# Optimization experiments

Measured on AMD Instinct MI355X. Metric: run time of the kernel, lower is better.

The kernel has to match this reference:

```python
import jax, jax.numpy as jnp
import numpy as np

NB_SAMPLES = 16
GAMMA = 0.04       # also the noise_intensity passed to randomArgmax
ALPHA = 1.0
EPS = 1e-10


def setup_inputs() -> dict:
    key = jax.random.key(0)
    k1, k2, k3 = jax.random.split(key, 3)
    B, H, W, K = 8, 128, 128, 32
    zbuf = jax.random.normal(k1, (B, H, W, K), dtype=jnp.float32)
    prob_map = jax.random.uniform(k2, (B, H, W, K), dtype=jnp.float32)
    mask = jnp.ones((B, H, W, K), dtype=jnp.float32)
    zfar = jnp.ones((1,), dtype=jnp.float32)
    znear = jnp.zeros((1,), dtype=jnp.float32)
    # gaussian noise normally drawn inside randomArgmax.forward; made explicit for determinism
    noise = jax.random.normal(k3, (NB_SAMPLES, B, H, W, K + 1), dtype=jnp.float32)
    return {"zbuf": zbuf, "zfar": zfar, "znear": znear,
            "prob_map": prob_map, "mask": mask, "noise": noise}


def _random_argmax(z, noise, sigma):
    # z: [B,H,W,C]; noise: [S,B,H,W,C]
    C = z.shape[-1]
    z_pert = z[None] + sigma * noise                       # [S,B,H,W,C]
    idx = jnp.argmax(z_pert, axis=-1)                      # first-max, matches torch.max
    weights = jax.nn.one_hot(idx, C, dtype=z.dtype)        # [S,B,H,W,C]
    return weights.mean(axis=0)                            # [B,H,W,C]


def reference(zbuf, zfar, znear, prob_map, mask, noise):
    # inverse depth, masked
    z_inv = (zfar - zbuf) / (zfar - znear) * mask          # [B,H,W,K]
    z_inv_max = jnp.maximum(jnp.max(z_inv, axis=-1, keepdims=True), EPS)
    z_map = GAMMA / ALPHA * jnp.log(1e-12 + prob_map) + z_inv - z_inv_max
    bg = EPS - z_inv_max                                   # background channel [B,H,W,1]
    z_map = jnp.concatenate([z_map, bg], axis=-1)          # [B,H,W,K+1]
    return _random_argmax(z_map, noise, GAMMA)
```

## Files before the change

kernel.cpp:

```cpp
#include <hip/hip_runtime.h>


#define NPIX   (8 * 128 * 128)
#define KCH    32
#define CCH    33
#define SAMP   16
#define TPB    256
#define TILE   (TPB * CCH)

#define GLL16(gp, lp)                                                     \
    __builtin_amdgcn_global_load_lds(                                     \
        (const __attribute__((address_space(1))) void*)(gp),              \
        (__attribute__((address_space(3))) void*)(lp), 16, 0, 0)

__device__ __forceinline__ void stage_tile(const float* __restrict__ gsrc,
                                           float* ldst, int tid)
{
    #pragma unroll
    for (int j = 0; j < (TILE / 4) / TPB; ++j) {
        const int i = tid + j * TPB;
        GLL16(gsrc + 4 * i, ldst + 4 * i);
    }
    if (tid < (TILE / 4) - ((TILE / 4) / TPB) * TPB) {
        const int i = tid + ((TILE / 4) / TPB) * TPB;
        GLL16(gsrc + 4 * i, ldst + 4 * i);
    }
}

__global__ __launch_bounds__(TPB)
void gauss_agg_kernel(const float* __restrict__ zbuf,
                      const float* __restrict__ zfar_p,
                      const float* __restrict__ znear_p,
                      const float* __restrict__ prob,
                      const float* __restrict__ mask,
                      const float* __restrict__ noise,
                      float* __restrict__ out)
{
#pragma clang fp contract(off)
    __shared__ float lds[2 * TILE];
    const int tid = threadIdx.x;
    const int p0  = blockIdx.x * TPB;
    const size_t p = (size_t)p0 + tid;

    stage_tile(noise + ((size_t)0 * NPIX + p0) * CCH, lds, tid);

    const float zfar  = zfar_p[0];
    const float znear = znear_p[0];
    const float denom = zfar - znear;

    float zb[KCH], pm[KCH], mk[KCH];
    {
        const float4* zb4 = reinterpret_cast<const float4*>(zbuf + p * KCH);
        const float4* pm4 = reinterpret_cast<const float4*>(prob + p * KCH);
        const float4* mk4 = reinterpret_cast<const float4*>(mask + p * KCH);
        #pragma unroll
        for (int i = 0; i < KCH / 4; ++i) {
            float4 a = zb4[i], b = pm4[i], c = mk4[i];
            zb[4*i+0] = a.x; zb[4*i+1] = a.y; zb[4*i+2] = a.z; zb[4*i+3] = a.w;
            pm[4*i+0] = b.x; pm[4*i+1] = b.y; pm[4*i+2] = b.z; pm[4*i+3] = b.w;
            mk[4*i+0] = c.x; mk[4*i+1] = c.y; mk[4*i+2] = c.z; mk[4*i+3] = c.w;
        }
    }

    float z_inv[KCH];
    float zmax = 1e-10f;
    #pragma unroll
    for (int k = 0; k < KCH; ++k) {
        float zi = ((zfar - zb[k]) / denom) * mk[k];
        z_inv[k] = zi;
        zmax = fmaxf(zmax, zi);
    }

    float z_map[CCH];
    #pragma unroll
    for (int k = 0; k < KCH; ++k) {
        float lg = logf(1e-12f + pm[k]);
        z_map[k] = ((0.04f * lg) + z_inv[k]) - zmax;
    }
    z_map[KCH] = 1e-10f - zmax;

    int acc[CCH];
    #pragma unroll
    for (int c = 0; c < CCH; ++c) acc[c] = 0;

    __syncthreads();

    for (int s = 0; s < SAMP; ++s) {
        if (s + 1 < SAMP)
            stage_tile(noise + ((size_t)(s + 1) * NPIX + p0) * CCH,
                       lds + ((s + 1) & 1) * TILE, tid);

        const float* cur = lds + (s & 1) * TILE;
        const int base = tid * CCH;
        float best = z_map[0] + (0.04f * cur[base + 0]);
        int bi = 0;
        #pragma unroll
        for (int c = 1; c < CCH; ++c) {
            float v = z_map[c] + (0.04f * cur[base + c]);
            if (v > best) { best = v; bi = c; }
        }
        #pragma unroll
        for (int c = 0; c < CCH; ++c) acc[c] += (bi == c) ? 1 : 0;

        __syncthreads();
    }

    {
        const int base = tid * CCH;
        #pragma unroll
        for (int c = 0; c < CCH; ++c)
            lds[base + c] = (float)acc[c] * 0.0625f;
    }
    __syncthreads();
    {
        const float4* l4 = reinterpret_cast<const float4*>(lds);
        float4* o4 = reinterpret_cast<float4*>(out + (size_t)p0 * CCH);
        for (int i = tid; i < TILE / 4; i += TPB) o4[i] = l4[i];
    }
}

extern "C" void kernel_launch(void* const* d_in, const int* in_sizes, int n_in,
                              void* d_out, int out_size, void* d_ws, size_t ws_size,
                              hipStream_t stream)
{
    const float* zbuf  = (const float*)d_in[0];
    const float* zfar  = (const float*)d_in[1];
    const float* znear = (const float*)d_in[2];
    const float* prob  = (const float*)d_in[3];
    const float* mask  = (const float*)d_in[4];
    const float* noise = (const float*)d_in[5];
    float* out = (float*)d_out;

    dim3 grid(NPIX / TPB), block(TPB);
    gauss_agg_kernel<<<grid, block, 0, stream>>>(zbuf, zfar, znear, prob, mask,
                                                 noise, out);
}
```

Baseline: 408.6 us.

## Stage noise per wavefront and replace block barriers with vmcnt waits

Each wavefront now double-buffers only the noise slice for its own 64 pixels into its own LDS region, instead of the whole block staging a shared tile. This lets the per-sample `__syncthreads` be replaced by an explicit `s_waitcnt vmcnt(9)`, which waits only for the previous stage's async global-to-LDS loads. The aim is to remove block-wide stalls so waves progress independently and overlap loads with the argmax. The risk is that correctness depends on the exact count of outstanding vector-memory instructions per stage.

```diff
diff --git a/kernel.cpp b/kernel.cpp
--- a/kernel.cpp
+++ b/kernel.cpp
@@ -7,24 +7,40 @@
 #define SAMP   16
 #define TPB    256
 #define TILE   (TPB * CCH)
+#define WFLOATS (64 * CCH)
 
 #define GLL16(gp, lp)                                                     \
     __builtin_amdgcn_global_load_lds(                                     \
         (const __attribute__((address_space(1))) void*)(gp),              \
         (__attribute__((address_space(3))) void*)(lp), 16, 0, 0)
 
-__device__ __forceinline__ void stage_tile(const float* __restrict__ gsrc,
-                                           float* ldst, int tid)
+__device__ __forceinline__ void stage_wave(const float* __restrict__ gsrc,
+                                           float* ldst, int lane)
 {
     #pragma unroll
-    for (int j = 0; j < (TILE / 4) / TPB; ++j) {
-        const int i = tid + j * TPB;
-        GLL16(gsrc + 4 * i, ldst + 4 * i);
+    for (int j = 0; j < 8; ++j) {
+        const int f = j * 64 + lane;
+        GLL16(gsrc + 4 * f, ldst + 4 * f);
     }
-    if (tid < (TILE / 4) - ((TILE / 4) / TPB) * TPB) {
-        const int i = tid + ((TILE / 4) / TPB) * TPB;
-        GLL16(gsrc + 4 * i, ldst + 4 * i);
+    if (lane < 16) {
+        const int f = 512 + lane;
+        GLL16(gsrc + 4 * f, ldst + 4 * f);
     }
+}
+
+__device__ __forceinline__ void argmax_sample(const float* __restrict__ cur,
+                                              const float* __restrict__ z_map,
+                                              int* __restrict__ acc, int base)
+{
+    float best = z_map[0] + (0.04f * cur[base + 0]);
+    int bi = 0;
+    #pragma unroll
+    for (int c = 1; c < CCH; ++c) {
+        float v = z_map[c] + (0.04f * cur[base + c]);
+        if (v > best) { best = v; bi = c; }
+    }
+    #pragma unroll
+    for (int c = 0; c < CCH; ++c) acc[c] += (bi == c) ? 1 : 0;
 }
 
 __global__ __launch_bounds__(TPB)
@@ -38,11 +54,13 @@
 {
 #pragma clang fp contract(off)
     __shared__ float lds[2 * TILE];
-    const int tid = threadIdx.x;
-    const int p0  = blockIdx.x * TPB;
+    const int tid  = threadIdx.x;
+    const int lane = tid & 63;
+    const int wsl  = (tid >> 6) * WFLOATS;
+    const int p0   = blockIdx.x * TPB;
     const size_t p = (size_t)p0 + tid;
 
-    stage_tile(noise + ((size_t)0 * NPIX + p0) * CCH, lds, tid);
+    stage_wave(noise + ((size_t)0 * NPIX + p0) * CCH + wsl, lds + wsl, lane);
 
     const float zfar  = zfar_p[0];
     const float znear = znear_p[0];
@@ -83,33 +101,26 @@
     #pragma unroll
     for (int c = 0; c < CCH; ++c) acc[c] = 0;
 
-    __syncthreads();
+    const int base = tid * CCH - wsl;
 
-    for (int s = 0; s < SAMP; ++s) {
-        if (s + 1 < SAMP)
-            stage_tile(noise + ((size_t)(s + 1) * NPIX + p0) * CCH,
-                       lds + ((s + 1) & 1) * TILE, tid);
-
-        const float* cur = lds + (s & 1) * TILE;
-        const int base = tid * CCH;
-        float best = z_map[0] + (0.04f * cur[base + 0]);
-        int bi = 0;
-        #pragma unroll
-        for (int c = 1; c < CCH; ++c) {
-            float v = z_map[c] + (0.04f * cur[base + c]);
-            if (v > best) { best = v; bi = c; }
-        }
-        #pragma unroll
-        for (int c = 0; c < CCH; ++c) acc[c] += (bi == c) ? 1 : 0;
-
-        __syncthreads();
+    for (int s = 0; s < SAMP - 1; ++s) {
+        stage_wave(noise + ((size_t)(s + 1) * NPIX + p0) * CCH + wsl,
+                   lds + ((s + 1) & 1) * TILE + wsl, lane);
+        asm volatile("s_waitcnt vmcnt(9)" ::: "memory");
+        const float* cur = lds + (s & 1) * TILE + wsl;
+        argmax_sample(cur, z_map, acc, base);
+    }
+    asm volatile("s_waitcnt vmcnt(0)" ::: "memory");
+    {
+        const float* cur = lds + ((SAMP - 1) & 1) * TILE + wsl;
+        argmax_sample(cur, z_map, acc, base);
     }
 
     {
-        const int base = tid * CCH;
+        const int b = tid * CCH;
         #pragma unroll
         for (int c = 0; c < CCH; ++c)
-            lds[base + c] = (float)acc[c] * 0.0625f;
+            lds[b + c] = (float)acc[c] * 0.0625f;
     }
     __syncthreads();
     {
```

New measurement: 408.2 us. Within noise of the previous version (-0.1%).
